# Performance work log

Hardware: AMD Instinct MI355X
Metric: run time of the kernel (lower is better)

The kernel has to match this reference:

```python
import jax, jax.numpy as jnp
import numpy as np

EPS = 1e-5  # torch BatchNorm1d default

def _silu(x):
    return x * jax.nn.sigmoid(x)

def _bn(x, g, b, rm, rv, axis):
    # eval-mode batchnorm along given channel axis
    shape = [1] * x.ndim
    shape[axis] = -1
    return (x - rm.reshape(shape)) * (g.reshape(shape) / jnp.sqrt(rv.reshape(shape) + EPS)) + b.reshape(shape)

def setup_inputs() -> dict:
    key = jax.random.key(0)
    ks = jax.random.split(key, 12)
    b, n, p, d, r = 64, 256, 12, 128, 2
    x = jax.random.normal(ks[0], (b, n, p, d), dtype=jnp.float32)
    # k branch: Conv1d(p -> 1, k=1, bias=False) + BN(1)
    wk = jax.random.normal(ks[1], (p,), dtype=jnp.float32) / np.sqrt(p)
    bn_k_g = jax.random.uniform(ks[2], (1,), dtype=jnp.float32, minval=0.5, maxval=1.5)
    bn_k_b = 0.1 * jax.random.normal(ks[3], (1,), dtype=jnp.float32)
    bn_k_rm = jnp.zeros((1,), jnp.float32)
    bn_k_rv = jnp.ones((1,), jnp.float32)
    # v branch: Conv1d(d -> d, k=1, bias=False) + BN(d)
    wv = jax.random.normal(ks[4], (d, d), dtype=jnp.float32) / np.sqrt(d)
    bn_v_g = jax.random.uniform(ks[5], (d,), dtype=jnp.float32, minval=0.5, maxval=1.5)
    bn_v_b = 0.1 * jax.random.normal(ks[6], (d,), dtype=jnp.float32)
    bn_v_rm = jnp.zeros((d,), jnp.float32)
    bn_v_rv = jnp.ones((d,), jnp.float32)
    # fc_avg / fc_max: Linear(n, n//r, bias=False) -> GELU -> Linear(n//r, n, bias=False)
    w_avg1 = jax.random.normal(ks[7], (n // r, n), dtype=jnp.float32) / np.sqrt(n)
    w_avg2 = jax.random.normal(ks[8], (n, n // r), dtype=jnp.float32) / np.sqrt(n // r)
    w_max1 = jax.random.normal(ks[9], (n // r, n), dtype=jnp.float32) / np.sqrt(n)
    w_max2 = jax.random.normal(ks[10], (n, n // r), dtype=jnp.float32) / np.sqrt(n // r)
    return dict(x=x, wk=wk, bn_k_g=bn_k_g, bn_k_b=bn_k_b, bn_k_rm=bn_k_rm, bn_k_rv=bn_k_rv,
                wv=wv, bn_v_g=bn_v_g, bn_v_b=bn_v_b, bn_v_rm=bn_v_rm, bn_v_rv=bn_v_rv,
                w_avg1=w_avg1, w_avg2=w_avg2, w_max1=w_max1, w_max2=w_max2)

def _forward(x, wk, bn_k_g, bn_k_b, bn_k_rm, bn_k_rv, wv, bn_v_g, bn_v_b, bn_v_rm, bn_v_rv,
             w_avg1, w_avg2, w_max1, w_max2):
    b, n, p, d = x.shape
    xf = x.reshape(b * n, p, d)
    # squeeze-excite gates: pool over d, FC over n
    avg = jnp.mean(xf, axis=-1).reshape(b, n, p).transpose(0, 2, 1)  # [b,p,n]
    mx = jnp.max(xf, axis=-1).reshape(b, n, p).transpose(0, 2, 1)    # [b,p,n]
    gelu = lambda t: jax.nn.gelu(t, approximate=False)
    avg_g = jax.nn.sigmoid(gelu(avg @ w_avg1.T) @ w_avg2.T).transpose(0, 2, 1)  # [b,n,p]
    max_g = jax.nn.sigmoid(gelu(mx @ w_max1.T) @ w_max2.T).transpose(0, 2, 1)   # [b,n,p]
    # k: 1x1 conv over p channels -> [bn, d], BN(1ch), SiLU, softmax over d
    k_raw = jnp.einsum('bpd,p->bd', xf, wk)
    k = jax.nn.softmax(_silu(k_raw * (bn_k_g / jnp.sqrt(bn_k_rv + EPS)) - bn_k_rm * (bn_k_g / jnp.sqrt(bn_k_rv + EPS)) + bn_k_b), axis=-1)  # [bn,d]
    # v: 1x1 conv over d channels on [bn,d,p], BN(d), SiLU -> [bn,p,d]
    v_raw = jnp.einsum('bpd,ed->bpe', xf, wv)  # channel axis is last here
    v = _silu(_bn(v_raw, bn_v_g, bn_v_b, bn_v_rm, bn_v_rv, axis=2))  # [bn,p,d]
    # y = v @ k : [bn,p];  y_pool = (max+avg) @ v : [bn,d]
    y = jnp.einsum('bpd,bd->bp', v, k)
    pool = (max_g + avg_g).reshape(b * n, p)
    y_pool = jnp.einsum('bp,bpd->bd', pool, v)
    out = y_pool[:, None, :] * y[:, :, None]  # [bn,p,d]
    return out.reshape(b, n, p, d)

def reference(x, wk, bn_k_g, bn_k_b, bn_k_rm, bn_k_rv, wv, bn_v_g, bn_v_b, bn_v_rm, bn_v_rv,
              w_avg1, w_avg2, w_max1, w_max2):
    return _forward(x, wk, bn_k_g, bn_k_b, bn_k_rm, bn_k_rv, wv, bn_v_g, bn_v_b, bn_v_rm, bn_v_rv,
                    w_avg1, w_avg2, w_max1, w_max2)
```

## Files before the change

kernel.cpp:

```cpp
#include <hip/hip_runtime.h>
#include <hip/hip_bf16.h>

#define B_   64
#define N_   256
#define P_   12
#define D_   128
#define BN_  (B_*N_)
#define EPSV 1e-5f
#define VST  130

typedef float  f32x4  __attribute__((ext_vector_type(4)));
typedef __bf16 bf16x8 __attribute__((ext_vector_type(8)));
typedef __bf16 bf16x4 __attribute__((ext_vector_type(4)));

__device__ float g_avg[768*256];
__device__ float g_mx [768*256];
__device__ float g_h1 [1536*128];
__device__ float g_pool[BN_*P_];

__device__ inline float sigm_(float x) { return 1.0f / (1.0f + __expf(-x)); }

__device__ inline float dot4_(float4 a, float4 b, float acc) {
  acc = fmaf(a.x, b.x, acc); acc = fmaf(a.y, b.y, acc);
  acc = fmaf(a.z, b.z, acc); acc = fmaf(a.w, b.w, acc);
  return acc;
}

__global__ __launch_bounds__(256) void k1_pool(const float* __restrict__ x) {
  int w = threadIdx.x >> 6, l = threadIdx.x & 63;
  int bn = blockIdx.x * 4 + w;
  const float* xp = x + (size_t)bn * (P_ * D_);
  int half = l >> 5, lane32 = l & 31;
  float s6[6], m6[6];
#pragma unroll
  for (int pp = 0; pp < 6; ++pp) {
    int p = pp * 2 + half;
    float4 v = *(const float4*)(xp + p * D_ + lane32 * 4);
    float s = (v.x + v.y) + (v.z + v.w);
    float m = fmaxf(fmaxf(v.x, v.y), fmaxf(v.z, v.w));
#pragma unroll
    for (int off = 16; off; off >>= 1) {
      s += __shfl_xor(s, off);
      m = fmaxf(m, __shfl_xor(m, off));
    }
    s6[pp] = s * (1.0f / D_);
    m6[pp] = m;
  }
  if (lane32 == 0) {
    int b = bn >> 8, n = bn & 255;
#pragma unroll
    for (int pp = 0; pp < 6; ++pp) {
      int p = pp * 2 + half;
      g_avg[(b * P_ + p) * N_ + n] = s6[pp];
      g_mx [(b * P_ + p) * N_ + n] = m6[pp];
    }
  }
}

__global__ __launch_bounds__(256) void k2_l1(const float* __restrict__ w_avg1,
                                             const float* __restrict__ w_max1) {
  __shared__ float in_t[16 * 256];
  __shared__ float w_t[64 * 68];
  int t = threadIdx.x;
  int rblk = blockIdx.x % 96, cblk = blockIdx.x / 96;
  int rr0 = rblk * 16, c0 = cblk * 64;
  bool mxb = (rr0 >= 768);
  int r768 = mxb ? rr0 - 768 : rr0;
  const float* in = (mxb ? g_mx : g_avg) + (size_t)r768 * 256;
  const float* w1 = mxb ? w_max1 : w_avg1;
#pragma unroll
  for (int i = 0; i < 4; ++i) {
    int F = t + i * 256, r = F >> 6, k4 = F & 63;
    *(float4*)(in_t + r * 256 + k4 * 4) = *(const float4*)(in + r * 256 + k4 * 4);
  }
  int c = t & 63, rq = t >> 6;
  float a0 = 0, a1 = 0, a2 = 0, a3 = 0;
  for (int kc = 0; kc < 4; ++kc) {
    __syncthreads();
#pragma unroll
    for (int i = 0; i < 4; ++i) {
      int F = t + i * 256, cr = F >> 4, k4 = F & 15;
      *(float4*)(w_t + cr * 68 + k4 * 4) =
          *(const float4*)(w1 + (size_t)(c0 + cr) * 256 + kc * 64 + k4 * 4);
    }
    __syncthreads();
#pragma unroll
    for (int k4 = 0; k4 < 16; ++k4) {
      float4 wv4 = *(float4*)(w_t + c * 68 + k4 * 4);
      a0 = dot4_(*(float4*)(in_t + (rq * 4 + 0) * 256 + kc * 64 + k4 * 4), wv4, a0);
      a1 = dot4_(*(float4*)(in_t + (rq * 4 + 1) * 256 + kc * 64 + k4 * 4), wv4, a1);
      a2 = dot4_(*(float4*)(in_t + (rq * 4 + 2) * 256 + kc * 64 + k4 * 4), wv4, a2);
      a3 = dot4_(*(float4*)(in_t + (rq * 4 + 3) * 256 + kc * 64 + k4 * 4), wv4, a3);
    }
  }
  float accs[4] = {a0, a1, a2, a3};
#pragma unroll
  for (int r = 0; r < 4; ++r) {
    float a = accs[r];
    float g = 0.5f * a * (1.0f + erff(a * 0.70710678f));
    g_h1[(size_t)(rr0 + rq * 4 + r) * 128 + c0 + c] = g;
  }
}

__global__ __launch_bounds__(256) void k2_l2(const float* __restrict__ w_avg2,
                                             const float* __restrict__ w_max2) {
  __shared__ float ina_t[16 * 128];
  __shared__ float inm_t[16 * 128];
  __shared__ float wa_t[64 * 68];
  __shared__ float wm_t[64 * 68];
  int t = threadIdx.x;
  int rblk = blockIdx.x % 48, cblk = blockIdx.x / 48;
  int rr0 = rblk * 16, n0 = cblk * 64;
#pragma unroll
  for (int i = 0; i < 2; ++i) {
    int F = t + i * 256, r = F >> 5, k4 = F & 31;
    *(float4*)(ina_t + r * 128 + k4 * 4) = *(const float4*)(g_h1 + (size_t)(rr0 + r) * 128 + k4 * 4);
    *(float4*)(inm_t + r * 128 + k4 * 4) = *(const float4*)(g_h1 + (size_t)(768 + rr0 + r) * 128 + k4 * 4);
  }
  int c = t & 63, rq = t >> 6;
  float aa0=0, aa1=0, aa2=0, aa3=0, am0=0, am1=0, am2=0, am3=0;
  for (int kc = 0; kc < 2; ++kc) {
    __syncthreads();
#pragma unroll
    for (int i = 0; i < 4; ++i) {
      int F = t + i * 256, cr = F >> 4, k4 = F & 15;
      *(float4*)(wa_t + cr * 68 + k4 * 4) =
          *(const float4*)(w_avg2 + (size_t)(n0 + cr) * 128 + kc * 64 + k4 * 4);
      *(float4*)(wm_t + cr * 68 + k4 * 4) =
          *(const float4*)(w_max2 + (size_t)(n0 + cr) * 128 + kc * 64 + k4 * 4);
    }
    __syncthreads();
#pragma unroll
    for (int k4 = 0; k4 < 16; ++k4) {
      float4 wa4 = *(float4*)(wa_t + c * 68 + k4 * 4);
      float4 wm4 = *(float4*)(wm_t + c * 68 + k4 * 4);
      float4 i0 = *(float4*)(ina_t + (rq * 4 + 0) * 128 + kc * 64 + k4 * 4);
      float4 i1 = *(float4*)(ina_t + (rq * 4 + 1) * 128 + kc * 64 + k4 * 4);
      float4 i2 = *(float4*)(ina_t + (rq * 4 + 2) * 128 + kc * 64 + k4 * 4);
      float4 i3 = *(float4*)(ina_t + (rq * 4 + 3) * 128 + kc * 64 + k4 * 4);
      aa0 = dot4_(i0, wa4, aa0); aa1 = dot4_(i1, wa4, aa1);
      aa2 = dot4_(i2, wa4, aa2); aa3 = dot4_(i3, wa4, aa3);
      float4 j0 = *(float4*)(inm_t + (rq * 4 + 0) * 128 + kc * 64 + k4 * 4);
      float4 j1 = *(float4*)(inm_t + (rq * 4 + 1) * 128 + kc * 64 + k4 * 4);
      float4 j2 = *(float4*)(inm_t + (rq * 4 + 2) * 128 + kc * 64 + k4 * 4);
      float4 j3 = *(float4*)(inm_t + (rq * 4 + 3) * 128 + kc * 64 + k4 * 4);
      am0 = dot4_(j0, wm4, am0); am1 = dot4_(j1, wm4, am1);
      am2 = dot4_(j2, wm4, am2); am3 = dot4_(j3, wm4, am3);
    }
  }
  float va[4] = {aa0, aa1, aa2, aa3};
  float vm[4] = {am0, am1, am2, am3};
#pragma unroll
  for (int r = 0; r < 4; ++r) {
    int rr = rr0 + rq * 4 + r;
    int b = rr / 12, p = rr % 12;
    float pv = sigm_(va[r]) + sigm_(vm[r]);
    g_pool[((size_t)b * 256 + (n0 + c)) * 12 + p] = pv;
  }
}

__global__ __launch_bounds__(256) void k3_main(
    const float* __restrict__ x,  const float* __restrict__ wk,
    const float* __restrict__ kg, const float* __restrict__ kb,
    const float* __restrict__ krm, const float* __restrict__ krv,
    const float* __restrict__ wv,
    const float* __restrict__ vg, const float* __restrict__ vb,
    const float* __restrict__ vrm, const float* __restrict__ vrv,
    float* __restrict__ out) {
  __shared__ __align__(16) __bf16 wv_lds[128 * 128];
  __shared__ float sv_l[128], tv_l[128];
  __shared__ float v_l[4][P_ * VST];

  int t = threadIdx.x, w = t >> 6, l = t & 63;
  if (t < 128) {
    float s = vg[t] * rsqrtf(vrv[t] + EPSV);
    sv_l[t] = s;
    tv_l[t] = vb[t] - vrm[t] * s;
  }
  __syncthreads();
  {
    int e = t >> 1, dh = (t & 1) * 64;
    float s = sv_l[e];
    int swz = (e & 7) << 4;
#pragma unroll
    for (int i = 0; i < 16; ++i) {
      float4 v4 = *(const float4*)(wv + (size_t)e * 128 + dh + i * 4);
      bf16x4 h;
      h[0] = (__bf16)(v4.x * s); h[1] = (__bf16)(v4.y * s);
      h[2] = (__bf16)(v4.z * s); h[3] = (__bf16)(v4.w * s);
      int byte = (e * 256 + (dh + i * 4) * 2) ^ swz;
      *(bf16x4*)((char*)wv_lds + byte) = h;
    }
  }
  float ksc = kg[0] * rsqrtf(krv[0] + EPSV);
  float kbs = kb[0] - krm[0] * ksc;
  __syncthreads();

  int arow = (l & 15) > 11 ? 11 : (l & 15);
  int ak = (l >> 4) * 8;
  int bcol = l & 15;
  int bko = (l >> 4) * 16;
  float* vw = &v_l[w][0];

  for (int it = 0; it < 4; ++it) {
    int bn = blockIdx.x * 16 + it * 4 + w;
    const float* xp = x + (size_t)bn * (P_ * D_);

    const float* pp = g_pool + (size_t)bn * 12;
    float pl[P_];
#pragma unroll
    for (int p = 0; p < P_; ++p) pl[p] = pp[p];

    bf16x8 afr[4];
#pragma unroll
    for (int ks = 0; ks < 4; ++ks) {
      const float* src = xp + arow * 128 + ks * 32 + ak;
      float4 lo = *(const float4*)(src);
      float4 hi = *(const float4*)(src + 4);
      bf16x8 a;
      a[0] = (__bf16)lo.x; a[1] = (__bf16)lo.y; a[2] = (__bf16)lo.z; a[3] = (__bf16)lo.w;
      a[4] = (__bf16)hi.x; a[5] = (__bf16)hi.y; a[6] = (__bf16)hi.z; a[7] = (__bf16)hi.w;
      afr[ks] = a;
    }

    float kr0 = 0, kr1 = 0;
#pragma unroll
    for (int p = 0; p < P_; ++p) {
      float2 xv = *(const float2*)(xp + p * 128 + 2 * l);
      float wkp = wk[p];
      kr0 = fmaf(xv.x, wkp, kr0);
      kr1 = fmaf(xv.y, wkp, kr1);
    }
    float z0 = kr0 * ksc + kbs, z1 = kr1 * ksc + kbs;
    z0 = z0 * sigm_(z0);
    z1 = z1 * sigm_(z1);
    float mmax = fmaxf(z0, z1);
#pragma unroll
    for (int off = 32; off; off >>= 1) mmax = fmaxf(mmax, __shfl_xor(mmax, off));
    float e0 = __expf(z0 - mmax), e1 = __expf(z1 - mmax);
    float es = e0 + e1;
#pragma unroll
    for (int off = 32; off; off >>= 1) es += __shfl_xor(es, off);
    float inv = 1.0f / es;
    float k0 = e0 * inv, k1 = e1 * inv;

    f32x4 acc[8];
#pragma unroll
    for (int nt = 0; nt < 8; ++nt) acc[nt] = (f32x4){0.f, 0.f, 0.f, 0.f};
#pragma unroll
    for (int nt = 0; nt < 8; ++nt) {
      int er = bcol + nt * 16;
      int base = er * 256;
      int sw = (er & 7) << 4;
#pragma unroll
      for (int ks = 0; ks < 4; ++ks) {
        int byte = (base + ks * 64 + bko) ^ sw;
        bf16x8 bfr = *(const bf16x8*)((const char*)wv_lds + byte);
        acc[nt] = __builtin_amdgcn_mfma_f32_16x16x32_bf16(afr[ks], bfr, acc[nt], 0, 0, 0);
      }
    }

    int p0 = (l >> 4) * 4;
    if (p0 < 12) {
#pragma unroll
      for (int nt = 0; nt < 8; ++nt) {
        int e = bcol + nt * 16;
        float tvv = tv_l[e];
#pragma unroll
        for (int r = 0; r < 4; ++r) {
          float a = acc[nt][r] + tvv;
          float v = a * sigm_(a);
          vw[(p0 + r) * VST + e] = v;
        }
      }
    }

    float yp0 = 0, yp1 = 0;
    float ypart[P_];
#pragma unroll
    for (int p = 0; p < P_; ++p) {
      float2 vvp = *(const float2*)(vw + p * VST + 2 * l);
      ypart[p] = vvp.x * k0 + vvp.y * k1;
      yp0 = fmaf(pl[p], vvp.x, yp0);
      yp1 = fmaf(pl[p], vvp.y, yp1);
    }
#pragma unroll
    for (int p = 0; p < P_; ++p) {
      float s = ypart[p];
#pragma unroll
      for (int off = 32; off; off >>= 1) s += __shfl_xor(s, off);
      ypart[p] = s;
    }
    float* op = out + (size_t)bn * (P_ * D_);
#pragma unroll
    for (int p = 0; p < P_; ++p) {
      float2 o;
      o.x = yp0 * ypart[p];
      o.y = yp1 * ypart[p];
      *(float2*)(op + p * 128 + 2 * l) = o;
    }
  }
}

extern "C" void kernel_launch(void* const* d_in, const int* in_sizes, int n_in,
                              void* d_out, int out_size, void* d_ws, size_t ws_size,
                              hipStream_t stream) {
  const float* x   = (const float*)d_in[0];
  const float* wk  = (const float*)d_in[1];
  const float* kg  = (const float*)d_in[2];
  const float* kbb = (const float*)d_in[3];
  const float* krm = (const float*)d_in[4];
  const float* krv = (const float*)d_in[5];
  const float* wvp = (const float*)d_in[6];
  const float* vg  = (const float*)d_in[7];
  const float* vbb = (const float*)d_in[8];
  const float* vrm = (const float*)d_in[9];
  const float* vrv = (const float*)d_in[10];
  const float* wa1 = (const float*)d_in[11];
  const float* wa2 = (const float*)d_in[12];
  const float* wm1 = (const float*)d_in[13];
  const float* wm2 = (const float*)d_in[14];
  float* out = (float*)d_out;

  k1_pool<<<4096, 256, 0, stream>>>(x);
  k2_l1<<<192, 256, 0, stream>>>(wa1, wm1);
  k2_l2<<<192, 256, 0, stream>>>(wa2, wm2);
  k3_main<<<1024, 256, 0, stream>>>(x, wk, kg, kbb, krm, krv, wvp, vg, vbb, vrm, vrv, out);
}
```

Baseline: 107.8 us.

## Compute y and y_pool directly from MFMA accumulators, drop V staging in LDS

The epilogue no longer writes the SiLU'd V tile to LDS and reads it back. It computes the per-row y dot products and the pool-weighted column sums straight from the MFMA accumulator layout, using lane shuffles within the 16-lane groups and across them. The softmax weights k are staged through a small per-wave LDS buffer so they can be re-read in the accumulator column order. Launch bounds now request 4 blocks per CU. The trade-off is that output stores become scalar strided writes of 16 consecutive floats per row segment instead of float2 full-row writes, and a quarter of the lanes (the padded rows) sit idle during the stores.

```diff
diff --git a/kernel.cpp b/kernel.cpp
--- a/kernel.cpp
+++ b/kernel.cpp
@@ -7,7 +7,6 @@
 #define D_   128
 #define BN_  (B_*N_)
 #define EPSV 1e-5f
-#define VST  130
 
 typedef float  f32x4  __attribute__((ext_vector_type(4)));
 typedef __bf16 bf16x8 __attribute__((ext_vector_type(8)));
@@ -159,7 +158,7 @@
   }
 }
 
-__global__ __launch_bounds__(256) void k3_main(
+__global__ __launch_bounds__(256, 4) void k3_main(
     const float* __restrict__ x,  const float* __restrict__ wk,
     const float* __restrict__ kg, const float* __restrict__ kb,
     const float* __restrict__ krm, const float* __restrict__ krv,
@@ -169,7 +168,7 @@
     float* __restrict__ out) {
   __shared__ __align__(16) __bf16 wv_lds[128 * 128];
   __shared__ float sv_l[128], tv_l[128];
-  __shared__ float v_l[4][P_ * VST];
+  __shared__ float k_lds[4][128];
 
   int t = threadIdx.x, w = t >> 6, l = t & 63;
   if (t < 128) {
@@ -200,16 +199,23 @@
   int ak = (l >> 4) * 8;
   int bcol = l & 15;
   int bko = (l >> 4) * 16;
-  float* vw = &v_l[w][0];
+  int p0 = (l >> 4) * 4;
+  bool rows_ok = (p0 < 12);
+
+  float tv_e[8];
+#pragma unroll
+  for (int nt = 0; nt < 8; ++nt) tv_e[nt] = tv_l[bcol + nt * 16];
 
   for (int it = 0; it < 4; ++it) {
     int bn = blockIdx.x * 16 + it * 4 + w;
     const float* xp = x + (size_t)bn * (P_ * D_);
 
-    const float* pp = g_pool + (size_t)bn * 12;
-    float pl[P_];
-#pragma unroll
-    for (int p = 0; p < P_; ++p) pl[p] = pp[p];
+    float pool_r[4] = {0.f, 0.f, 0.f, 0.f};
+    if (rows_ok) {
+      const float* pp = g_pool + (size_t)bn * 12 + p0;
+#pragma unroll
+      for (int r = 0; r < 4; ++r) pool_r[r] = pp[r];
+    }
 
     bf16x8 afr[4];
 #pragma unroll
@@ -242,7 +248,12 @@
 #pragma unroll
     for (int off = 32; off; off >>= 1) es += __shfl_xor(es, off);
     float inv = 1.0f / es;
-    float k0 = e0 * inv, k1 = e1 * inv;
+
+    float2 kw; kw.x = e0 * inv; kw.y = e1 * inv;
+    *(float2*)(&k_lds[w][2 * l]) = kw;
+    float k_e[8];
+#pragma unroll
+    for (int nt = 0; nt < 8; ++nt) k_e[nt] = k_lds[w][bcol + nt * 16];
 
     f32x4 acc[8];
 #pragma unroll
@@ -260,44 +271,40 @@
       }
     }
 
-    int p0 = (l >> 4) * 4;
-    if (p0 < 12) {
-#pragma unroll
-      for (int nt = 0; nt < 8; ++nt) {
-        int e = bcol + nt * 16;
-        float tvv = tv_l[e];
-#pragma unroll
-        for (int r = 0; r < 4; ++r) {
-          float a = acc[nt][r] + tvv;
-          float v = a * sigm_(a);
-          vw[(p0 + r) * VST + e] = v;
+    float y_r[4] = {0.f, 0.f, 0.f, 0.f};
+    float ypp[8];
+#pragma unroll
+    for (int nt = 0; nt < 8; ++nt) {
+      float s = 0.f;
+#pragma unroll
+      for (int r = 0; r < 4; ++r) {
+        float a = acc[nt][r] + tv_e[nt];
+        float v = a * sigm_(a);
+        y_r[r] = fmaf(v, k_e[nt], y_r[r]);
+        s = fmaf(pool_r[r], v, s);
+      }
+      ypp[nt] = s;
+    }
+#pragma unroll
+    for (int r = 0; r < 4; ++r) {
+#pragma unroll
+      for (int off = 8; off; off >>= 1) y_r[r] += __shfl_xor(y_r[r], off);
+    }
+#pragma unroll
+    for (int nt = 0; nt < 8; ++nt) {
+      ypp[nt] += __shfl_xor(ypp[nt], 16);
+      ypp[nt] += __shfl_xor(ypp[nt], 32);
+    }
+
+    if (rows_ok) {
+      float* op = out + (size_t)bn * (P_ * D_) + p0 * 128 + bcol;
+#pragma unroll
+      for (int r = 0; r < 4; ++r) {
+#pragma unroll
+        for (int nt = 0; nt < 8; ++nt) {
+          op[r * 128 + nt * 16] = y_r[r] * ypp[nt];
         }
       }
-    }
-
-    float yp0 = 0, yp1 = 0;
-    float ypart[P_];
-#pragma unroll
-    for (int p = 0; p < P_; ++p) {
-      float2 vvp = *(const float2*)(vw + p * VST + 2 * l);
-      ypart[p] = vvp.x * k0 + vvp.y * k1;
-      yp0 = fmaf(pl[p], vvp.x, yp0);
-      yp1 = fmaf(pl[p], vvp.y, yp1);
-    }
-#pragma unroll
-    for (int p = 0; p < P_; ++p) {
-      float s = ypart[p];
-#pragma unroll
-      for (int off = 32; off; off >>= 1) s += __shfl_xor(s, off);
-      ypart[p] = s;
-    }
-    float* op = out + (size_t)bn * (P_ * D_);
-#pragma unroll
-    for (int p = 0; p < P_; ++p) {
-      float2 o;
-      o.x = yp0 * ypart[p];
-      o.y = yp1 * ypart[p];
-      *(float2*)(op + p * 128 + 2 * l) = o;
     }
   }
 }
```

Result: slower. 176.4 us (+63.6%).
